# Kernel optimization log

Measured on AMD Instinct MI355X. Metric: run time of the kernel, lower is better.

Reference implementation:

```python
import jax, jax.numpy as jnp
import numpy as np

EPS = 1e-6
D = 100   # embed_dim
P = 10    # perspective


def _cos(v1, v2):
    # cosine over last dim with broadcasting; clamp sum-of-squares at EPS (as torch)
    num = (v1 * v2).sum(-1)
    n1 = jnp.sqrt(jnp.clip((v1 * v1).sum(-1), EPS, None))
    n2 = jnp.sqrt(jnp.clip((v2 * v2).sum(-1), EPS, None))
    return num / (n1 * n2)


def _cosine_matrix(s1, s2):
    # [n1,B,D] x [n2,B,D] -> [n1,n2,B]; einsum avoids the [n1,n2,B,D] intermediate
    num = jnp.einsum('ibd,jbd->ijb', s1, s2)
    n1 = jnp.sqrt(jnp.clip((s1 * s1).sum(-1), EPS, None))  # [n1,B]
    n2 = jnp.sqrt(jnp.clip((s2 * s2).sum(-1), EPS, None))  # [n2,B]
    return num / (n1[:, None] * n2[None])


def _full(s1, s2, w):
    ws1 = s1[:, :, None, :] * w            # [n1,B,P,D]
    ws2 = s2[-1][:, None, :] * w           # [B,P,D]
    return _cos(ws1, ws2[None])            # [n1,B,P]


def _maxpool(s1, s2, w):
    # cos[i,j,b,p] between s1[i,b]*w[p] and s2[j,b]*w[p], without the 5-D intermediate
    w2 = w * w
    num = jnp.einsum('ibd,jbd,pd->ijbp', s1, s2, w2)
    n1 = jnp.sqrt(jnp.clip(jnp.einsum('ibd,pd->ibp', s1 * s1, w2), EPS, None))
    n2 = jnp.sqrt(jnp.clip(jnp.einsum('jbd,pd->jbp', s2 * s2, w2), EPS, None))
    cos = num / (n1[:, None] * n2[None])
    return cos.max(1)                      # [n1,B,P]


def _mean_att(s1, s2, w, cosm):
    # attentive vector: cosine-weighted mean of s2 states -> [n1,B,D]
    att = jnp.einsum('ijb,jbd->ibd', cosm, s2) / (cosm.sum(1) + EPS)[..., None]
    return _cos(s1[:, :, None, :] * w, att[:, :, None, :] * w)


def _max_att(s1, s2, w, cosm):
    n1, B = cosm.shape[0], s2.shape[1]
    idx = jnp.argmax(cosm, axis=1).reshape(-1)  # values in [0, n_state2)
    # NOTE: faithful to the torch source, which indexes the flattened [n2*B, D]
    # view of s2 with per-state indices (a bug in the original, reproduced here).
    att = s2.reshape(-1, D)[idx].reshape(n1, B, D)
    return _cos(s1[:, :, None, :] * w, att[:, :, None, :] * w)


def setup_inputs() -> dict:
    key = jax.random.key(0)
    ks = jax.random.split(key, 10)
    s1 = jax.random.normal(ks[0], (100, 256, 2 * D), dtype=jnp.float32)
    s2 = jax.random.normal(ks[1], (100, 256, 2 * D), dtype=jnp.float32)
    ws = {f'w{i+1}': jax.random.uniform(ks[2 + i], (P, D), dtype=jnp.float32,
                                        minval=-0.01, maxval=0.01) for i in range(8)}
    return {'s1': s1, 's2': s2, **ws}


def reference(s1, s2, w1, w2, w3, w4, w5, w6, w7, w8):
    s1f, s1b = s1[..., :D], s1[..., D:]
    s2f, s2b = s2[..., :D], s2[..., D:]
    cosf = _cosine_matrix(s1f, s2f)
    cosb = _cosine_matrix(s1b, s2b)
    full = jnp.concatenate([_full(s1f, s2f, w1), _full(s1b, s2b, w2)], 2)
    maxp = jnp.concatenate([_maxpool(s1f, s2f, w3), _maxpool(s1b, s2b, w4)], 2)
    mean_a = jnp.concatenate([_mean_att(s1f, s2f, w5, cosf), _mean_att(s1b, s2b, w6, cosb)], 2)
    # original forward uses mean_attentive for the backward half of max-attentive (bug kept)
    max_a = jnp.concatenate([_max_att(s1f, s2f, w7, cosf), _mean_att(s1b, s2b, w8, cosb)], 2)
    # `type` in the original forward shadows the builtin, so the 'all' branch always runs
    return jnp.concatenate([full, maxp, mean_a, max_a], axis=-1)  # [n1,B,8P]
```

## Files before the change

### kernel.cpp

```cpp
#include <hip/hip_runtime.h>

#define TT 100
#define DD 100
#define DC 25
#define PP 10
#define BBATCH 256
#define OC 80
#define NW 8
#define NR 2

typedef float v2f __attribute__((ext_vector_type(2)));
typedef float v4f __attribute__((ext_vector_type(4)));

static constexpr float FEPS = 1e-6f;

__device__ __forceinline__ int   f2i(float x) { return __builtin_bit_cast(int, x); }
__device__ __forceinline__ float i2f(int x)   { return __builtin_bit_cast(float, x); }

#define ROR_F(v, ctrl) i2f(__builtin_amdgcn_update_dpp(0, f2i(v), (ctrl), 0xf, 0xf, false))
#define ROR_I(v, ctrl) __builtin_amdgcn_update_dpp(0, (v), (ctrl), 0xf, 0xf, false)

__device__ __forceinline__ v2f xswap32_f(float v) {
#if __has_builtin(__builtin_amdgcn_permlane32_swap)
  auto pr = __builtin_amdgcn_permlane32_swap((unsigned)f2i(v), (unsigned)f2i(v), false, false);
  v2f r; r.x = i2f((int)pr[0]); r.y = i2f((int)pr[1]);
  return r;
#else
  v2f r; r.x = v; r.y = __shfl_xor(v, 32, 64);
  return r;
#endif
}

__device__ __forceinline__ float wave_sum(float v) {
  v += ROR_F(v, 0x121);
  v += ROR_F(v, 0x122);
  v += ROR_F(v, 0x124);
  v += ROR_F(v, 0x128);
  v += i2f(__builtin_amdgcn_ds_swizzle(f2i(v), 0x401f));
  v2f s = xswap32_f(v);
  return s.x + s.y;
}

__device__ __forceinline__ float wave_max(float v) {
  v = fmaxf(v, ROR_F(v, 0x121));
  v = fmaxf(v, ROR_F(v, 0x122));
  v = fmaxf(v, ROR_F(v, 0x124));
  v = fmaxf(v, ROR_F(v, 0x128));
  v = fmaxf(v, i2f(__builtin_amdgcn_ds_swizzle(f2i(v), 0x401f)));
  v2f s = xswap32_f(v);
  return fmaxf(s.x, s.y);
}

__device__ __forceinline__ void amax2(float& v, int& i, float ov, int oi) {
  if (ov > v || (ov == v && oi < i)) { v = ov; i = oi; }
}

__device__ __forceinline__ void wave_argmax(float& v, int& idx) {
  amax2(v, idx, ROR_F(v, 0x121), ROR_I(idx, 0x121));
  amax2(v, idx, ROR_F(v, 0x122), ROR_I(idx, 0x122));
  amax2(v, idx, ROR_F(v, 0x124), ROR_I(idx, 0x124));
  amax2(v, idx, ROR_F(v, 0x128), ROR_I(idx, 0x128));
  amax2(v, idx, i2f(__builtin_amdgcn_ds_swizzle(f2i(v), 0x401f)),
        __builtin_amdgcn_ds_swizzle(idx, 0x401f));
#if __has_builtin(__builtin_amdgcn_permlane32_swap)
  {
    auto rv = __builtin_amdgcn_permlane32_swap((unsigned)f2i(v), (unsigned)f2i(v), false, false);
    auto ri = __builtin_amdgcn_permlane32_swap((unsigned)idx, (unsigned)idx, false, false);
    amax2(v, idx, i2f((int)rv[0]), (int)ri[0]);
    amax2(v, idx, i2f((int)rv[1]), (int)ri[1]);
  }
#else
  amax2(v, idx, __shfl_xor(v, 32, 64), __shfl_xor(idx, 32, 64));
#endif
}

__global__ __launch_bounds__(512, 2) void match_kernel(
    const float* __restrict__ s1, const float* __restrict__ s2,
    const float* __restrict__ w1, const float* __restrict__ w2,
    const float* __restrict__ w3, const float* __restrict__ w4,
    const float* __restrict__ w5, const float* __restrict__ w6,
    const float* __restrict__ w7, const float* __restrict__ w8,
    float* __restrict__ out)
{
  const int dir  = blockIdx.x & 1;
  const int b    = blockIdx.x >> 1;
  const int doff = dir * DD;
  const int tid  = threadIdx.x;
  const int lane = tid & 63;
  const int wv   = tid >> 6;

  const float* wfull = dir ? w2 : w1;
  const float* wmax  = dir ? w4 : w3;
  const float* wmean = dir ? w6 : w5;
  const float* watt2 = dir ? w8 : w7;

  __shared__ __align__(16) float S2V[DC][TT + 1][4];
  __shared__ __align__(16) float W2SQ[PP][DD];
  __shared__ __align__(16) float W2T[DC][4][PP];
  __shared__ float N2PI[TT];
  __shared__ float N2WI[TT][11];
  __shared__ __align__(16) float S1R[NR * NW][DD];
  __shared__ __align__(16) float CROW[NR * NW][DD];
  __shared__ float N1PI[NR * NW];
  __shared__ float N1WI[NR * NW][PP];
  __shared__ int   ARGJ[NR * NW];

  for (int idx = tid; idx < TT * DD; idx += 512) {
    int j = idx / DD, d = idx - j * DD;
    S2V[d >> 2][j][d & 3] = s2[(j * BBATCH + b) * (2 * DD) + doff + d];
  }
  for (int idx = tid; idx < PP * DD; idx += 512) {
    int p = idx / DD, d = idx - p * DD;
    float v = wmax[idx];
    float v2 = v * v;
    W2SQ[p][d] = v2;
    W2T[d >> 2][d & 3][p] = v2;
  }
  __syncthreads();

  for (int task = tid; task < TT + TT * PP; task += 512) {
    if (task < TT) {
      int j = task;
      float a = 0.f;
      for (int c = 0; c < DC; ++c) {
        v4f f = *(const v4f*)&S2V[c][j][0];
#pragma unroll
        for (int k = 0; k < 4; ++k) a = fmaf(f[k], f[k], a);
      }
      N2PI[j] = 1.0f / sqrtf(fmaxf(a, FEPS));
    } else {
      int q = task - TT; int j = q / PP, p = q - j * PP;
      float a = 0.f;
      for (int c = 0; c < DC; ++c) {
        v4f f = *(const v4f*)&S2V[c][j][0];
        v4f w = *(const v4f*)&W2SQ[p][4 * c];
#pragma unroll
        for (int k = 0; k < 4; ++k) a = fmaf(f[k] * f[k], w[k], a);
      }
      N2WI[j][p] = rsqrtf(fmaxf(a, FEPS));
    }
  }
  __syncthreads();

  const int  j0   = lane;
  const int  j1   = 64 + lane;
  const bool act1 = (j1 < TT);
  const int  j1c  = act1 ? j1 : (TT - 1);
  const bool actd = (64 + lane) < DD;
  const int  d1   = actd ? (64 + lane) : (DD - 1);
  const int  c0i  = lane >> 2, k0 = lane & 3;
  const int  c1i  = d1 >> 2,   k1 = d1 & 3;

  const int sl = wv * NR;

  for (int g = wv; g < 50; g += NW) {
    const int i0 = g * NR;

    if (lane < NR * DC) {
      int rr = lane / DC, c = lane - rr * DC;
      *(v4f*)&S1R[sl + rr][4 * c] =
          *(const v4f*)&s1[((i0 + rr) * BBATCH + b) * (2 * DD) + doff + 4 * c];
    }

    if (lane < NR * 11) {
      int rr = lane / 11, q = lane - rr * 11;
      if (q == 0) {
        float a = 0.f;
        for (int c = 0; c < DC; ++c) {
          v4f f = *(const v4f*)&S1R[sl + rr][4 * c];
#pragma unroll
          for (int k = 0; k < 4; ++k) a = fmaf(f[k], f[k], a);
        }
        N1PI[sl + rr] = 1.0f / sqrtf(fmaxf(a, FEPS));
      } else {
        int p = q - 1;
        float a = 0.f;
        for (int c = 0; c < DC; ++c) {
          v4f f = *(const v4f*)&S1R[sl + rr][4 * c];
          v4f w = *(const v4f*)&W2SQ[p][4 * c];
#pragma unroll
          for (int k = 0; k < 4; ++k) a = fmaf(f[k] * f[k], w[k], a);
        }
        N1WI[sl + rr][p] = rsqrtf(fmaxf(a, FEPS));
      }
    }

    float rs[NR] = {0, 0};
    v2f attp[NR] = {{0, 0}, {0, 0}};

    float dot0[NR] = {0, 0};
    float dot1[NR] = {0, 0};
    v2f wap[NR][2][5];
#pragma unroll
    for (int r = 0; r < NR; ++r)
#pragma unroll
      for (int pp = 0; pp < 5; ++pp) {
        wap[r][0][pp] = (v2f){0.f, 0.f};
        wap[r][1][pp] = (v2f){0.f, 0.f};
      }

    for (int c = 0; c < DC; ++c) {
      v4f s2a4 = *(const v4f*)&S2V[c][j0][0];
      v4f s2b4 = *(const v4f*)&S2V[c][j1c][0];
      v4f s1v[NR];
#pragma unroll
      for (int r = 0; r < NR; ++r) s1v[r] = *(const v4f*)&S1R[sl + r][4 * c];
#pragma unroll
      for (int k = 0; k < 4; ++k) {
        v4f wA = *(const v4f*)&W2T[c][k][0];
        v4f wB = *(const v4f*)&W2T[c][k][4];
        v2f wp4 = *(const v2f*)&W2T[c][k][8];
        v2f wp0 = __builtin_shufflevector(wA, wA, 0, 1);
        v2f wp1 = __builtin_shufflevector(wA, wA, 2, 3);
        v2f wp2 = __builtin_shufflevector(wB, wB, 0, 1);
        v2f wp3 = __builtin_shufflevector(wB, wB, 2, 3);
#pragma unroll
        for (int r = 0; r < NR; ++r) {
          float ta0 = s1v[r][k] * s2a4[k];
          float ta1 = s1v[r][k] * s2b4[k];
          dot0[r] += ta0;
          dot1[r] += ta1;
          v2f t0; t0.x = ta0; t0.y = ta0;
          v2f t1; t1.x = ta1; t1.y = ta1;
          wap[r][0][0] = __builtin_elementwise_fma(t0, wp0, wap[r][0][0]);
          wap[r][0][1] = __builtin_elementwise_fma(t0, wp1, wap[r][0][1]);
          wap[r][0][2] = __builtin_elementwise_fma(t0, wp2, wap[r][0][2]);
          wap[r][0][3] = __builtin_elementwise_fma(t0, wp3, wap[r][0][3]);
          wap[r][0][4] = __builtin_elementwise_fma(t0, wp4, wap[r][0][4]);
          wap[r][1][0] = __builtin_elementwise_fma(t1, wp0, wap[r][1][0]);
          wap[r][1][1] = __builtin_elementwise_fma(t1, wp1, wap[r][1][1]);
          wap[r][1][2] = __builtin_elementwise_fma(t1, wp2, wap[r][1][2]);
          wap[r][1][3] = __builtin_elementwise_fma(t1, wp3, wap[r][1][3]);
          wap[r][1][4] = __builtin_elementwise_fma(t1, wp4, wap[r][1][4]);
        }
      }
    }

#pragma unroll
    for (int r = 0; r < NR; ++r) {
      float n1pi_r = N1PI[sl + r];
      float c0 = dot0[r] * (n1pi_r * N2PI[j0]);
      float c1 = dot1[r] * (n1pi_r * N2PI[j1c]);
      CROW[sl + r][j0] = c0;
      if (act1) CROW[sl + r][j1] = c1;
      rs[r] = wave_sum(c0 + (act1 ? c1 : 0.f));

      float mv = c0; int mi = j0;
      if (act1 && (c1 > mv)) { mv = c1; mi = j1; }
      wave_argmax(mv, mi);
      if (lane == 0) ARGJ[sl + r] = mi;

#pragma unroll
      for (int p = 0; p < PP; ++p) {
        float a0 = (p & 1) ? wap[r][0][p >> 1].y : wap[r][0][p >> 1].x;
        float a1 = (p & 1) ? wap[r][1][p >> 1].y : wap[r][1][p >> 1].x;
        float v0 = a0 * N2WI[j0][p];
        float v1 = act1 ? a1 * N2WI[j1c][p] : -3.4e38f;
        float m = wave_max(fmaxf(v0, v1));
        if (lane == 0) {
          out[((i0 + r) * BBATCH + b) * OC + 20 + dir * PP + p] = m * N1WI[sl + r][p];
        }
      }
    }

    for (int j = 0; j < TT; ++j) {
      v2f s2ab; s2ab.x = S2V[c0i][j][k0]; s2ab.y = S2V[c1i][j][k1];
#pragma unroll
      for (int r = 0; r < NR; ++r) {
        float cv = CROW[sl + r][j];
        v2f cc; cc.x = cv; cc.y = cv;
        attp[r] = __builtin_elementwise_fma(cc, s2ab, attp[r]);
      }
    }

#pragma unroll
    for (int r = 0; r < NR; ++r) {
      float inv = 1.0f / (rs[r] + FEPS);
      CROW[sl + r][lane] = attp[r].x * inv;
      if (actd) CROW[sl + r][64 + lane] = attp[r].y * inv;
    }

    if (lane < NR * 30) {
      int tk = lane;
      int r = tk / 30;
      int q = tk - r * 30;
      int set = q / PP;
      int p = q - set * PP;
      const float* wrow = (set == 0 ? wfull : (set == 1 ? wmean : watt2)) + p * DD;
      const float* gat = s2 + ARGJ[sl + r] * (2 * DD);
      float num = 0.f, nx = 0.f, ny = 0.f;
      for (int c = 0; c < DC; ++c) {
        v4f x4 = *(const v4f*)&S1R[sl + r][4 * c];
        v4f y4;
        if (set == 0)                     y4 = *(const v4f*)&S2V[c][TT - 1][0];
        else if (set == 1 || dir == 1)    y4 = *(const v4f*)&CROW[sl + r][4 * c];
        else                              y4 = *(const v4f*)&gat[4 * c];
        v4f w4 = *(const v4f*)&wrow[4 * c];
#pragma unroll
        for (int k = 0; k < 4; ++k) {
          float w2v = w4[k] * w4[k];
          num = fmaf(x4[k] * y4[k], w2v, num);
          nx  = fmaf(x4[k] * x4[k], w2v, nx);
          ny  = fmaf(y4[k] * y4[k], w2v, ny);
        }
      }
      float cres = num * rsqrtf(fmaxf(nx, FEPS)) * rsqrtf(fmaxf(ny, FEPS));
      int ch = (set == 0 ? 0 : (set == 1 ? 40 : 60)) + dir * PP + p;
      out[((i0 + r) * BBATCH + b) * OC + ch] = cres;
    }
  }
}

extern "C" void kernel_launch(void* const* d_in, const int* in_sizes, int n_in,
                              void* d_out, int out_size, void* d_ws, size_t ws_size,
                              hipStream_t stream) {
  const float* s1 = (const float*)d_in[0];
  const float* s2 = (const float*)d_in[1];
  match_kernel<<<dim3(512), dim3(512), 0, stream>>>(
      s1, s2,
      (const float*)d_in[2], (const float*)d_in[3],
      (const float*)d_in[4], (const float*)d_in[5],
      (const float*)d_in[6], (const float*)d_in[7],
      (const float*)d_in[8], (const float*)d_in[9],
      (float*)d_out);
}
```

Before: 409.3 us.

## Compute maxpool weighted cosine numerators with fp16 MFMA in shared memory

The per-perspective weighted dot products for the maxpool matching, previously accumulated with scalar FMAs inside the main per-row loop, are now computed in a separate phase with 16x16x32 fp16 MFMA over padded fp16 copies of s1, s2 and scaled squared weights. Row maxima are reduced with DPP and stored in shared memory, then scaled by the norms at output time. This removes most of the VALU work and register pressure from the inner loop. In exchange it uses fp16 inputs with a large weight scale, which risks precision loss, and it adds a lot of shared memory that may lower occupancy.

```diff
diff --git a/kernel.cpp b/kernel.cpp
--- a/kernel.cpp
+++ b/kernel.cpp
@@ -11,8 +11,11 @@
 
 typedef float v2f __attribute__((ext_vector_type(2)));
 typedef float v4f __attribute__((ext_vector_type(4)));
+typedef _Float16 f16x8 __attribute__((ext_vector_type(8)));
 
 static constexpr float FEPS = 1e-6f;
+static constexpr float WSCALE   = 16777216.f;
+static constexpr float WSCALE_I = 5.9604644775390625e-8f;
 
 __device__ __forceinline__ int   f2i(float x) { return __builtin_bit_cast(int, x); }
 __device__ __forceinline__ float i2f(int x)   { return __builtin_bit_cast(float, x); }
@@ -39,16 +42,6 @@
   v += i2f(__builtin_amdgcn_ds_swizzle(f2i(v), 0x401f));
   v2f s = xswap32_f(v);
   return s.x + s.y;
-}
-
-__device__ __forceinline__ float wave_max(float v) {
-  v = fmaxf(v, ROR_F(v, 0x121));
-  v = fmaxf(v, ROR_F(v, 0x122));
-  v = fmaxf(v, ROR_F(v, 0x124));
-  v = fmaxf(v, ROR_F(v, 0x128));
-  v = fmaxf(v, i2f(__builtin_amdgcn_ds_swizzle(f2i(v), 0x401f)));
-  v2f s = xswap32_f(v);
-  return fmaxf(s.x, s.y);
 }
 
 __device__ __forceinline__ void amax2(float& v, int& i, float ov, int oi) {
@@ -95,26 +88,43 @@
   const float* watt2 = dir ? w8 : w7;
 
   __shared__ __align__(16) float S2V[DC][TT + 1][4];
+  __shared__ __align__(16) _Float16 S1H[112][136];
+  __shared__ __align__(16) _Float16 S2H[112][136];
+  __shared__ __align__(16) _Float16 W2H[PP][136];
   __shared__ __align__(16) float W2SQ[PP][DD];
-  __shared__ __align__(16) float W2T[DC][4][PP];
   __shared__ float N2PI[TT];
   __shared__ float N2WI[TT][11];
+  __shared__ float RMAXL[TT][11];
   __shared__ __align__(16) float S1R[NR * NW][DD];
   __shared__ __align__(16) float CROW[NR * NW][DD];
   __shared__ float N1PI[NR * NW];
   __shared__ float N1WI[NR * NW][PP];
   __shared__ int   ARGJ[NR * NW];
 
-  for (int idx = tid; idx < TT * DD; idx += 512) {
-    int j = idx / DD, d = idx - j * DD;
-    S2V[d >> 2][j][d & 3] = s2[(j * BBATCH + b) * (2 * DD) + doff + d];
-  }
-  for (int idx = tid; idx < PP * DD; idx += 512) {
-    int p = idx / DD, d = idx - p * DD;
-    float v = wmax[idx];
-    float v2 = v * v;
-    W2SQ[p][d] = v2;
-    W2T[d >> 2][d & 3][p] = v2;
+  for (int idx = tid; idx < 112 * 136; idx += 512) {
+    int i = idx / 136, d = idx - i * 136;
+    float v = 0.f;
+    if (i < TT && d < DD) {
+      v = s2[(i * BBATCH + b) * (2 * DD) + doff + d];
+      S2V[d >> 2][i][d & 3] = v;
+    }
+    S2H[i][d] = (_Float16)v;
+  }
+  for (int idx = tid; idx < 112 * 136; idx += 512) {
+    int i = idx / 136, d = idx - i * 136;
+    float v = 0.f;
+    if (i < TT && d < DD) v = s1[(i * BBATCH + b) * (2 * DD) + doff + d];
+    S1H[i][d] = (_Float16)v;
+  }
+  for (int idx = tid; idx < PP * 136; idx += 512) {
+    int p = idx / 136, d = idx - p * 136;
+    float v2 = 0.f;
+    if (d < DD) {
+      float w = wmax[p * DD + d];
+      v2 = w * w;
+      W2SQ[p][d] = v2;
+    }
+    W2H[p][d] = (_Float16)(v2 * WSCALE);
   }
   __syncthreads();
 
@@ -138,6 +148,54 @@
         for (int k = 0; k < 4; ++k) a = fmaf(f[k] * f[k], w[k], a);
       }
       N2WI[j][p] = rsqrtf(fmaxf(a, FEPS));
+    }
+  }
+  __syncthreads();
+
+  {
+    const int fi = lane & 15;
+    const int ke = (lane >> 4) << 3;
+    for (int t = wv; t < 70; t += NW) {
+      int p  = t / 7;
+      int it = t - p * 7;
+      const int li = it * 16 + fi;
+      f16x8 aw[4];
+#pragma unroll
+      for (int ks = 0; ks < 4; ++ks)
+        aw[ks] = *(const f16x8*)&S1H[li][ks * 32 + ke] *
+                 *(const f16x8*)&W2H[p][ks * 32 + ke];
+      v4f rmax = {-3.4e38f, -3.4e38f, -3.4e38f, -3.4e38f};
+      for (int jt = 0; jt < 7; ++jt) {
+        const int lj = jt * 16 + fi;
+        v4f acc = {0.f, 0.f, 0.f, 0.f};
+#pragma unroll
+        for (int ks = 0; ks < 4; ++ks)
+          acc = __builtin_amdgcn_mfma_f32_16x16x32_f16(
+              aw[ks], *(const f16x8*)&S2H[lj][ks * 32 + ke], acc, 0, 0, 0);
+        const bool jok = lj < TT;
+        const float sc = N2WI[jok ? lj : 0][p];
+#pragma unroll
+        for (int r = 0; r < 4; ++r) {
+          float v = acc[r] * sc;
+          rmax[r] = fmaxf(rmax[r], jok ? v : -3.4e38f);
+        }
+      }
+#pragma unroll
+      for (int r = 0; r < 4; ++r) {
+        float m = rmax[r];
+        m = fmaxf(m, ROR_F(m, 0x121));
+        m = fmaxf(m, ROR_F(m, 0x122));
+        m = fmaxf(m, ROR_F(m, 0x124));
+        m = fmaxf(m, ROR_F(m, 0x128));
+        rmax[r] = m;
+      }
+      if (fi == 0) {
+#pragma unroll
+        for (int r = 0; r < 4; ++r) {
+          int i = it * 16 + ((lane >> 4) << 2) + r;
+          if (i < TT) RMAXL[i][p] = rmax[r];
+        }
+      }
     }
   }
   __syncthreads();
@@ -190,15 +248,6 @@
 
     float dot0[NR] = {0, 0};
     float dot1[NR] = {0, 0};
-    v2f wap[NR][2][5];
-#pragma unroll
-    for (int r = 0; r < NR; ++r)
-#pragma unroll
-      for (int pp = 0; pp < 5; ++pp) {
-        wap[r][0][pp] = (v2f){0.f, 0.f};
-        wap[r][1][pp] = (v2f){0.f, 0.f};
-      }
-
     for (int c = 0; c < DC; ++c) {
       v4f s2a4 = *(const v4f*)&S2V[c][j0][0];
       v4f s2b4 = *(const v4f*)&S2V[c][j1c][0];
@@ -207,31 +256,12 @@
       for (int r = 0; r < NR; ++r) s1v[r] = *(const v4f*)&S1R[sl + r][4 * c];
 #pragma unroll
       for (int k = 0; k < 4; ++k) {
-        v4f wA = *(const v4f*)&W2T[c][k][0];
-        v4f wB = *(const v4f*)&W2T[c][k][4];
-        v2f wp4 = *(const v2f*)&W2T[c][k][8];
-        v2f wp0 = __builtin_shufflevector(wA, wA, 0, 1);
-        v2f wp1 = __builtin_shufflevector(wA, wA, 2, 3);
-        v2f wp2 = __builtin_shufflevector(wB, wB, 0, 1);
-        v2f wp3 = __builtin_shufflevector(wB, wB, 2, 3);
 #pragma unroll
         for (int r = 0; r < NR; ++r) {
           float ta0 = s1v[r][k] * s2a4[k];
           float ta1 = s1v[r][k] * s2b4[k];
           dot0[r] += ta0;
           dot1[r] += ta1;
-          v2f t0; t0.x = ta0; t0.y = ta0;
-          v2f t1; t1.x = ta1; t1.y = ta1;
-          wap[r][0][0] = __builtin_elementwise_fma(t0, wp0, wap[r][0][0]);
-          wap[r][0][1] = __builtin_elementwise_fma(t0, wp1, wap[r][0][1]);
-          wap[r][0][2] = __builtin_elementwise_fma(t0, wp2, wap[r][0][2]);
-          wap[r][0][3] = __builtin_elementwise_fma(t0, wp3, wap[r][0][3]);
-          wap[r][0][4] = __builtin_elementwise_fma(t0, wp4, wap[r][0][4]);
-          wap[r][1][0] = __builtin_elementwise_fma(t1, wp0, wap[r][1][0]);
-          wap[r][1][1] = __builtin_elementwise_fma(t1, wp1, wap[r][1][1]);
-          wap[r][1][2] = __builtin_elementwise_fma(t1, wp2, wap[r][1][2]);
-          wap[r][1][3] = __builtin_elementwise_fma(t1, wp3, wap[r][1][3]);
-          wap[r][1][4] = __builtin_elementwise_fma(t1, wp4, wap[r][1][4]);
         }
       }
     }
@@ -250,16 +280,9 @@
       wave_argmax(mv, mi);
       if (lane == 0) ARGJ[sl + r] = mi;
 
-#pragma unroll
-      for (int p = 0; p < PP; ++p) {
-        float a0 = (p & 1) ? wap[r][0][p >> 1].y : wap[r][0][p >> 1].x;
-        float a1 = (p & 1) ? wap[r][1][p >> 1].y : wap[r][1][p >> 1].x;
-        float v0 = a0 * N2WI[j0][p];
-        float v1 = act1 ? a1 * N2WI[j1c][p] : -3.4e38f;
-        float m = wave_max(fmaxf(v0, v1));
-        if (lane == 0) {
-          out[((i0 + r) * BBATCH + b) * OC + 20 + dir * PP + p] = m * N1WI[sl + r][p];
-        }
+      if (lane < PP) {
+        out[((i0 + r) * BBATCH + b) * OC + 20 + dir * PP + lane] =
+            RMAXL[i0 + r][lane] * N1WI[sl + r][lane] * WSCALE_I;
       }
     }
 
```

Result: slower. 633.0 us (+54.7%).
